# Performance work log

Measured on AMD Instinct MI355X. Metric: run time of the kernel, lower is better.

Reference implementation:

```python
import jax, jax.numpy as jnp
import numpy as np

B, C, H, W = 8, 256, 32, 32
N_HEAD, D_K, D_V, OUT_C = 8, 32, 32, 256


def _relative_indices(height, width):
    # idx[i, j] = (y_j - y_i + H) * W + (x_j - x_i + W), matching the torch loop
    ys, xs = np.meshgrid(np.arange(height), np.arange(width), indexing='ij')
    ys, xs = ys.reshape(-1), xs.reshape(-1)  # [L]
    rel_y = ys[None, :] - ys[:, None] + height  # [L, L]
    rel_x = xs[None, :] - xs[:, None] + width
    return jnp.asarray(rel_y * width + rel_x, dtype=jnp.int32)


def setup_inputs() -> dict:
    key = jax.random.key(0)
    ks = jax.random.split(key, 7)
    sc = lambda fan_in: 1.0 / np.sqrt(fan_in)
    table = ((2 * H - 1) * (2 * W - 1))  # 3969
    return {
        'x': jax.random.normal(ks[0], (B, C, H, W), jnp.float32),
        'Qw': jax.random.normal(ks[1], (C, N_HEAD * D_K), jnp.float32) * sc(C),
        'Kw': jax.random.normal(ks[2], (C, N_HEAD * D_K), jnp.float32) * sc(C),
        'Vw': jax.random.normal(ks[3], (C, N_HEAD * D_V), jnp.float32) * sc(C),
        'ffw': jax.random.normal(ks[4], (N_HEAD * D_V, OUT_C), jnp.float32) * sc(N_HEAD * D_V),
        'ffb': jax.random.normal(ks[5], (OUT_C,), jnp.float32) * 0.01,
        'rel_bias': jax.random.normal(ks[6], (N_HEAD, table), jnp.float32),
        'rel_idx': _relative_indices(H, W),  # [L, L] int32
    }


def reference(x, Qw, Kw, Vw, ffw, ffb, rel_bias, rel_idx):
    b, c, h_, w_ = x.shape
    L = h_ * w_
    nh = rel_bias.shape[0]
    dk = Qw.shape[1] // nh
    dv = Vw.shape[1] // nh
    xf = x.reshape(b, c, L).transpose(0, 2, 1)  # [b, L, c]
    q = (xf @ Qw).reshape(b, L, nh, dk).transpose(0, 2, 1, 3)  # [b, h, L, dk]
    k = (xf @ Kw).reshape(b, L, nh, dk).transpose(0, 2, 1, 3)
    v = (xf @ Vw).reshape(b, L, nh, dv).transpose(0, 2, 1, 3)
    bias = rel_bias[:, rel_idx]  # gather -> [h, L, L]
    sim = jnp.einsum('bhid,bhjd->bhij', q, k) + bias[None]  # no 1/sqrt(dk) in original
    attn = jax.nn.softmax(sim, axis=-1)  # dropout is identity in eval
    out = jnp.einsum('bhij,bhjd->bhid', attn, v)  # [b, h, L, dv]
    out = out.transpose(0, 2, 1, 3).reshape(b, L, nh * dv)
    out = out @ ffw + ffb  # [b, L, out_c]
    return out.transpose(0, 2, 1).reshape(b, -1, h_, w_)
```

## Files before the change

kernel.cpp:

```cpp
#include <hip/hip_runtime.h>
#include <math.h>


typedef unsigned short u16;
typedef __bf16 bf16;
typedef bf16 bf16x8 __attribute__((ext_vector_type(8)));
typedef bf16 bf16x4 __attribute__((ext_vector_type(4)));
typedef short s16x4 __attribute__((ext_vector_type(4)));
typedef float f32x4 __attribute__((ext_vector_type(4)));
typedef float f32x4u __attribute__((ext_vector_type(4), aligned(4)));
typedef u16 u16x8 __attribute__((ext_vector_type(8)));
typedef u16 u16x4 __attribute__((ext_vector_type(4)));

#define DEVI __device__ __forceinline__

DEVI u16 bfbits(float f) { return __builtin_bit_cast(u16, (bf16)f); }

DEVI void async_cp16(const u16* g, u16* l) {
    __builtin_amdgcn_global_load_lds((const __attribute__((address_space(1))) void*)g,
                                     (__attribute__((address_space(3))) void*)l, 16, 0, 0);
}

DEVI f32x4 pv_mfma(bf16x4 a, bf16x4 b, f32x4 c) {
#if __has_builtin(__builtin_amdgcn_mfma_f32_16x16x16bf16_1k)
    return __builtin_amdgcn_mfma_f32_16x16x16bf16_1k(
        __builtin_bit_cast(s16x4, a), __builtin_bit_cast(s16x4, b), c, 0, 0, 0);
#else
    asm("s_nop 1\n\tv_mfma_f32_16x16x16_bf16 %0, %1, %2, %0"
        : "+v"(c) : "v"(a), "v"(b));
    return c;
#endif
}

__global__ __launch_bounds__(256) void prep(const float* __restrict__ X,
                                            const float* __restrict__ Qw, const float* __restrict__ Kw,
                                            const float* __restrict__ Vw, const float* __restrict__ Fw,
                                            const float* __restrict__ RB,
                                            u16* __restrict__ XF, u16* __restrict__ WT,
                                            float* __restrict__ RBs) {
    __shared__ u16 t[64 * 65];
    const int blk = blockIdx.x, tid = threadIdx.x;
    if (blk < 576) {
        const float* src;
        int cbase, rbase, rows_total;
        u16* dst;
        if (blk < 512) {
            const int b = blk >> 6;
            cbase = (blk & 3) * 64; rbase = ((blk >> 2) & 15) * 64;
            src = X + (size_t)b * 256 * 1024; dst = XF + (size_t)b * 1024 * 256;
            rows_total = 1024;
        } else {
            const int t2 = blk - 512, wsel = t2 >> 4;
            cbase = (t2 & 3) * 64; rbase = ((t2 >> 2) & 3) * 64;
            src = wsel == 0 ? Qw : wsel == 1 ? Kw : wsel == 2 ? Vw : Fw;
            dst = WT + (size_t)wsel * 256 * 256;
            rows_total = 256;
        }
        const int w = tid >> 6, r = tid & 63;
#pragma unroll
        for (int i = 0; i < 16; i++) {
            const int c = w * 16 + i;
            t[c * 65 + r] = bfbits(src[(size_t)(cbase + c) * rows_total + rbase + r]);
        }
        __syncthreads();
#pragma unroll
        for (int i = 0; i < 2; i++) {
            const int idx = i * 256 + tid;
            const int r2 = idx >> 3, cg = idx & 7;
            u16x8 v;
#pragma unroll
            for (int j = 0; j < 8; j++) v[j] = t[(cg * 8 + j) * 65 + r2];
            *(u16x8*)&dst[(size_t)(rbase + r2) * 256 + cbase + cg * 8] = v;
        }
    } else {
        const int n = 8 * 3969;
        for (int i = (blk - 576) * 256 + tid; i < n; i += 32 * 256)
            RBs[i] = RB[i] * 1.44269504f;
    }
}

template <int MFR, int PASS>
__global__ __launch_bounds__(256, 3) void gemm_fused(const u16* __restrict__ xf, const u16* __restrict__ wt,
                                                     u16* __restrict__ q, u16* __restrict__ kk,
                                                     u16* __restrict__ vt, const u16* __restrict__ ob,
                                                     float* __restrict__ outf, const float* __restrict__ ffb) {
    constexpr int TM = MFR * 32;
    __shared__ __align__(16) u16 lA[TM * 32];
    __shared__ __align__(16) u16 lB[64 * 32];
    const int tid = threadIdx.x;
    const int wave = tid >> 6, lane = tid & 63;
    const int quad = lane >> 4, l15 = lane & 15;

    int mode, mbase, nbase;
    const u16 *A, *Bt;
    if (PASS == 2) {
        mode = 2; A = wt + 768 * 256; Bt = ob;
        mbase = (blockIdx.x & 3) * 64; nbase = (blockIdx.x >> 2) * 64;
    } else if (blockIdx.x < 512) {
        mode = 0; A = xf; Bt = wt;
        mbase = (blockIdx.x >> 3) * TM; nbase = (blockIdx.x & 7) * 64;
    } else {
        mode = 1; A = wt + 512 * 256; Bt = xf;
        const int t = blockIdx.x - 512;
        mbase = (t & 1) * TM; nbase = (t >> 1) * 64;
    }

    const int m0 = (wave >> 1) * (MFR * 16), n0 = (wave & 1) * 32;
    const int srow = tid >> 2;
    const int sgcol = (lane & 3) ^ ((lane >> 3) & 3);
    const int kcol = ((quad ^ ((l15 >> 1) & 3))) * 8;

    f32x4 acc[MFR][2];
#pragma unroll
    for (int i = 0; i < MFR; i++)
#pragma unroll
        for (int j = 0; j < 2; j++) acc[i][j] = f32x4{0.f, 0.f, 0.f, 0.f};

    for (int kb = 0; kb < 256; kb += 32) {
        __syncthreads();
#pragma unroll
        for (int half = 0; half < MFR / 2; half++)
            async_cp16(&A[(size_t)(mbase + half * 64 + srow) * 256 + kb + sgcol * 8],
                       &lA[half * 2048 + wave * 512]);
        async_cp16(&Bt[(size_t)(nbase + srow) * 256 + kb + sgcol * 8], &lB[wave * 512]);
        __syncthreads();
        bf16x8 af[MFR], bfr[2];
#pragma unroll
        for (int i = 0; i < MFR; i++) af[i] = *(const bf16x8*)&lA[(m0 + i * 16 + l15) * 32 + kcol];
#pragma unroll
        for (int j = 0; j < 2; j++) bfr[j] = *(const bf16x8*)&lB[(n0 + j * 16 + l15) * 32 + kcol];
#pragma unroll
        for (int i = 0; i < MFR; i++)
#pragma unroll
            for (int j = 0; j < 2; j++)
                acc[i][j] = __builtin_amdgcn_mfma_f32_16x16x32_bf16(af[i], bfr[j], acc[i][j], 0, 0, 0);
    }

#pragma unroll
    for (int i = 0; i < MFR; i++) {
#pragma unroll
        for (int j = 0; j < 2; j++) {
#pragma unroll
            for (int r = 0; r < 4; r++) {
                const int gm = mbase + m0 + i * 16 + quad * 4 + r;
                const int gn = nbase + n0 + j * 16 + l15;
                float v = acc[i][j][r];
                if (mode == 0) {
                    const int b = gm >> 10, l = gm & 1023;
                    int n = gn;
                    u16* dst = q;
                    if (n >= 256) { n -= 256; dst = kk; }
                    else v *= 1.44269504f;
                    const int h = n >> 5, d = n & 31;
                    dst[(((size_t)(b * 8 + h) * 1024 + l) << 5) + d] = bfbits(v);
                } else if (mode == 1) {
                    const int h = gm >> 5, d = gm & 31;
                    const int b = gn >> 10, l = gn & 1023;
                    vt[(((size_t)(b * 8 + h) * 32 + d) << 10) + l] = bfbits(v);
                } else {
                    const int b = gn >> 10, l = gn & 1023;
                    outf[(((size_t)(b * 256 + gm)) << 10) + l] = v + ffb[gm];
                }
            }
        }
    }
}

__global__ __launch_bounds__(256, 2) void attn(const u16* __restrict__ Q, const u16* __restrict__ Kb,
                                               const u16* __restrict__ Vt, const float* __restrict__ RBs,
                                               u16* __restrict__ O) {
    __shared__ __align__(16) u16 kbuf[4][2][32 * 32];
    __shared__ __align__(16) u16 vbuf[4][2][32 * 32];
    const int tid = threadIdx.x;
    const int wave = tid >> 6, lane = tid & 63;
    const int quad = lane >> 4, l15 = lane & 15;
    const int blk = blockIdx.x;
    const int bh = ((blk >> 6) << 3) + (blk & 7);
    const int qt = (blk >> 3) & 7;
    const int b = bh >> 3, h = bh & 7;
    const int qbase = qt * 128 + wave * 32;
    const size_t bhL = (size_t)bh * 1024;

    const bf16x8 qfA = *(const bf16x8*)&Q[(bhL + qbase + l15) * 32 + quad * 8];
    const bf16x8 qfB = *(const bf16x8*)&Q[(bhL + qbase + 16 + l15) * 32 + quad * 8];
    const float* brow0 = RBs + (size_t)h * 3969
                         + (32 - (qbase >> 5)) * 32 + 32 - l15 + quad * 4;
    const int srow = lane >> 2;
    const int sgcol = (lane & 3) ^ ((lane >> 3) & 3);
    const u16* ksrc = &Kb[bhL * 32];
    const u16* vsrc_lo = &Vt[(((size_t)bh * 32) + srow) << 10];
    const u16* vsrc_hi = &Vt[(((size_t)bh * 32) + 16 + srow) << 10];

    float lsumA = 0.f, lsumB = 0.f;
    f32x4 oA_lo{0.f, 0.f, 0.f, 0.f}, oA_hi{0.f, 0.f, 0.f, 0.f};
    f32x4 oB_lo{0.f, 0.f, 0.f, 0.f}, oB_hi{0.f, 0.f, 0.f, 0.f};

    const int swz = (l15 >> 1) & 3;
    const int kcol = (quad ^ swz) * 8;
    const int g0 = (2 * ((quad >> 1) ^ swz) + (quad & 1)) * 4;
    const int g1 = (2 * (((quad >> 1) + 2) ^ swz) + (quad & 1)) * 4;

#define STAGE(buf, c) do {                                                              \
        const int kb_ = (c) * 32;                                                       \
        async_cp16(ksrc + kb_ * 32 + srow * 32 + sgcol * 8, &kbuf[wave][buf][0]);       \
        async_cp16(ksrc + kb_ * 32 + 512 + srow * 32 + sgcol * 8, &kbuf[wave][buf][512]); \
        async_cp16(vsrc_lo + kb_ + sgcol * 8, &vbuf[wave][buf][0]);                     \
        async_cp16(vsrc_hi + kb_ + sgcol * 8, &vbuf[wave][buf][512]);                   \
    } while (0)

#define COMPUTE(cur, c) do {                                                              \
        const bf16x8 kf0 = *(const bf16x8*)&kbuf[wave][cur][l15 * 32 + kcol];             \
        const bf16x8 kf1 = *(const bf16x8*)&kbuf[wave][cur][(16 + l15) * 32 + kcol];      \
        const bf16x4 v00 = __builtin_bit_cast(bf16x4, *(const u16x4*)&vbuf[wave][cur][l15 * 32 + g0]); \
        const bf16x4 v10 = __builtin_bit_cast(bf16x4, *(const u16x4*)&vbuf[wave][cur][l15 * 32 + g1]); \
        const bf16x4 v01 = __builtin_bit_cast(bf16x4, *(const u16x4*)&vbuf[wave][cur][(16 + l15) * 32 + g0]); \
        const bf16x4 v11 = __builtin_bit_cast(bf16x4, *(const u16x4*)&vbuf[wave][cur][(16 + l15) * 32 + g1]); \
        const f32x4u bm = *(const f32x4u*)(brow0 + (c) * 32 - 16);                        \
        const f32x4u b0 = *(const f32x4u*)(brow0 + (c) * 32);                             \
        const f32x4u b1 = *(const f32x4u*)(brow0 + (c) * 32 + 16);                        \
        const f32x4 z{0.f, 0.f, 0.f, 0.f};                                                \
        f32x4 s0A = __builtin_amdgcn_mfma_f32_16x16x32_bf16(kf0, qfA, z, 0, 0, 0);        \
        f32x4 s1A = __builtin_amdgcn_mfma_f32_16x16x32_bf16(kf1, qfA, z, 0, 0, 0);        \
        f32x4 s0B = __builtin_amdgcn_mfma_f32_16x16x32_bf16(kf0, qfB, z, 0, 0, 0);        \
        f32x4 s1B = __builtin_amdgcn_mfma_f32_16x16x32_bf16(kf1, qfB, z, 0, 0, 0);        \
        bf16x4 p0A, p1A, p0B, p1B;                                                        \
        float lsA = 0.f, lsB = 0.f;                                                       \
        _Pragma("unroll")                                                                 \
        for (int r = 0; r < 4; r++) {                                                     \
            const float e0A = __builtin_amdgcn_exp2f(s0A[r] + b0[r]);                     \
            const float e1A = __builtin_amdgcn_exp2f(s1A[r] + b1[r]);                     \
            const float e0B = __builtin_amdgcn_exp2f(s0B[r] + bm[r]);                     \
            const float e1B = __builtin_amdgcn_exp2f(s1B[r] + b0[r]);                     \
            lsA += e0A + e1A; lsB += e0B + e1B;                                           \
            p0A[r] = (bf16)e0A; p1A[r] = (bf16)e1A;                                       \
            p0B[r] = (bf16)e0B; p1B[r] = (bf16)e1B;                                       \
        }                                                                                 \
        lsumA += lsA; lsumB += lsB;                                                       \
        oA_lo = pv_mfma(p0A, v00, oA_lo);                                                 \
        oA_hi = pv_mfma(p0A, v01, oA_hi);                                                 \
        oA_lo = pv_mfma(p1A, v10, oA_lo);                                                 \
        oA_hi = pv_mfma(p1A, v11, oA_hi);                                                 \
        oB_lo = pv_mfma(p0B, v00, oB_lo);                                                 \
        oB_hi = pv_mfma(p0B, v01, oB_hi);                                                 \
        oB_lo = pv_mfma(p1B, v10, oB_lo);                                                 \
        oB_hi = pv_mfma(p1B, v11, oB_hi);                                                 \
    } while (0)

#define WAIT4 asm volatile("s_waitcnt vmcnt(4)" ::: "memory")
#define WAIT0 asm volatile("s_waitcnt vmcnt(0)" ::: "memory")
#define DSDRAIN asm volatile("s_waitcnt lgkmcnt(0)" ::: "memory")

    STAGE(0, 0);
    STAGE(1, 1);
    for (int c = 0; c < 28; c += 2) {
        WAIT4; COMPUTE(0, c);     DSDRAIN; STAGE(0, c + 2);
        WAIT4; COMPUTE(1, c + 1); DSDRAIN; STAGE(1, c + 3);
    }
    WAIT4; COMPUTE(0, 28); DSDRAIN; STAGE(0, 30);
    WAIT4; COMPUTE(1, 29); DSDRAIN; STAGE(1, 31);
    WAIT4; COMPUTE(0, 30);
    WAIT0; COMPUTE(1, 31);
#undef STAGE
#undef COMPUTE
#undef WAIT4
#undef WAIT0
#undef DSDRAIN

    lsumA += __shfl_xor(lsumA, 16);
    lsumA += __shfl_xor(lsumA, 32);
    lsumB += __shfl_xor(lsumB, 16);
    lsumB += __shfl_xor(lsumB, 32);
#pragma unroll
    for (int r = 0; r < 4; r++) {
        const float invA = 1.f / __shfl(lsumA, quad * 4 + r);
        const float invB = 1.f / __shfl(lsumB, quad * 4 + r);
        const int iA = qbase + quad * 4 + r;
        const int iB = iA + 16;
        O[((size_t)(b * 1024 + iA) * 256) + h * 32 + l15] = bfbits(oA_lo[r] * invA);
        O[((size_t)(b * 1024 + iA) * 256) + h * 32 + 16 + l15] = bfbits(oA_hi[r] * invA);
        O[((size_t)(b * 1024 + iB) * 256) + h * 32 + l15] = bfbits(oB_lo[r] * invB);
        O[((size_t)(b * 1024 + iB) * 256) + h * 32 + 16 + l15] = bfbits(oB_hi[r] * invB);
    }
}

extern "C" void kernel_launch(void* const* d_in, const int* in_sizes, int n_in,
                              void* d_out, int out_size, void* d_ws, size_t ws_size,
                              hipStream_t stream) {
    const float* x   = (const float*)d_in[0];
    const float* Qw  = (const float*)d_in[1];
    const float* Kw  = (const float*)d_in[2];
    const float* Vw  = (const float*)d_in[3];
    const float* Fw  = (const float*)d_in[4];
    const float* ffb = (const float*)d_in[5];
    const float* RB  = (const float*)d_in[6];

    u16* ws = (u16*)d_ws;
    u16* xf = ws;
    u16* wt = xf + 2097152;
    u16* q  = wt + 262144;
    u16* kk = q  + 2097152;
    u16* vt = kk + 2097152;
    float* RBs = (float*)(vt + 2097152);
    u16* ob = xf;

    prep<<<dim3(608), 256, 0, stream>>>(x, Qw, Kw, Vw, Fw, RB, xf, wt, RBs);
    gemm_fused<4, 0><<<dim3(768), 256, 0, stream>>>(xf, wt, q, kk, vt, nullptr, nullptr, nullptr);
    attn<<<dim3(512), 256, 0, stream>>>(q, kk, vt, RBs, ob);
    gemm_fused<2, 2><<<dim3(512), 256, 0, stream>>>(xf, wt, q, kk, vt, ob, (float*)d_out, ffb);
}
```

Baseline: 117.8 us.

## Split attention key range across two wave groups and merge partials in LDS

The attention block grows from 4 to 8 waves. Each query-subtile pair of waves handles half of the 32 key chunks, and the two halves combine their output accumulators and row sums through shared memory before the final normalisation and store. This doubles the waves working on each block, adding latency hiding and parallelism for the short 512-block grid. In exchange it doubles LDS staging buffers, adds two barriers and a reduction, and each wave runs a shorter pipeline. The merge is valid without max-tracking because the softmax is computed without a running max (plain exp sums).

```diff
diff --git a/kernel.cpp b/kernel.cpp
--- a/kernel.cpp
+++ b/kernel.cpp
@@ -166,19 +166,20 @@
     }
 }
 
-__global__ __launch_bounds__(256, 2) void attn(const u16* __restrict__ Q, const u16* __restrict__ Kb,
+__global__ __launch_bounds__(512, 4) void attn(const u16* __restrict__ Q, const u16* __restrict__ Kb,
                                                const u16* __restrict__ Vt, const float* __restrict__ RBs,
                                                u16* __restrict__ O) {
-    __shared__ __align__(16) u16 kbuf[4][2][32 * 32];
-    __shared__ __align__(16) u16 vbuf[4][2][32 * 32];
+    __shared__ __align__(16) u16 kbuf[8][2][32 * 32];
+    __shared__ __align__(16) u16 vbuf[8][2][32 * 32];
     const int tid = threadIdx.x;
     const int wave = tid >> 6, lane = tid & 63;
     const int quad = lane >> 4, l15 = lane & 15;
+    const int qsub = wave & 3, half = wave >> 2;
     const int blk = blockIdx.x;
     const int bh = ((blk >> 6) << 3) + (blk & 7);
     const int qt = (blk >> 3) & 7;
     const int b = bh >> 3, h = bh & 7;
-    const int qbase = qt * 128 + wave * 32;
+    const int qbase = qt * 128 + qsub * 32;
     const size_t bhL = (size_t)bh * 1024;
 
     const bf16x8 qfA = *(const bf16x8*)&Q[(bhL + qbase + l15) * 32 + quad * 8];
@@ -250,16 +251,17 @@
 #define WAIT0 asm volatile("s_waitcnt vmcnt(0)" ::: "memory")
 #define DSDRAIN asm volatile("s_waitcnt lgkmcnt(0)" ::: "memory")
 
-    STAGE(0, 0);
-    STAGE(1, 1);
-    for (int c = 0; c < 28; c += 2) {
+    const int c0 = half * 16;
+    STAGE(0, c0);
+    STAGE(1, c0 + 1);
+    for (int c = c0; c < c0 + 12; c += 2) {
         WAIT4; COMPUTE(0, c);     DSDRAIN; STAGE(0, c + 2);
         WAIT4; COMPUTE(1, c + 1); DSDRAIN; STAGE(1, c + 3);
     }
-    WAIT4; COMPUTE(0, 28); DSDRAIN; STAGE(0, 30);
-    WAIT4; COMPUTE(1, 29); DSDRAIN; STAGE(1, 31);
-    WAIT4; COMPUTE(0, 30);
-    WAIT0; COMPUTE(1, 31);
+    WAIT4; COMPUTE(0, c0 + 12); DSDRAIN; STAGE(0, c0 + 14);
+    WAIT4; COMPUTE(1, c0 + 13); DSDRAIN; STAGE(1, c0 + 15);
+    WAIT4; COMPUTE(0, c0 + 14);
+    WAIT0; COMPUTE(1, c0 + 15);
 #undef STAGE
 #undef COMPUTE
 #undef WAIT4
@@ -270,16 +272,37 @@
     lsumA += __shfl_xor(lsumA, 32);
     lsumB += __shfl_xor(lsumB, 16);
     lsumB += __shfl_xor(lsumB, 32);
-#pragma unroll
-    for (int r = 0; r < 4; r++) {
-        const float invA = 1.f / __shfl(lsumA, quad * 4 + r);
-        const float invB = 1.f / __shfl(lsumB, quad * 4 + r);
-        const int iA = qbase + quad * 4 + r;
-        const int iB = iA + 16;
-        O[((size_t)(b * 1024 + iA) * 256) + h * 32 + l15] = bfbits(oA_lo[r] * invA);
-        O[((size_t)(b * 1024 + iA) * 256) + h * 32 + 16 + l15] = bfbits(oA_hi[r] * invA);
-        O[((size_t)(b * 1024 + iB) * 256) + h * 32 + l15] = bfbits(oB_lo[r] * invB);
-        O[((size_t)(b * 1024 + iB) * 256) + h * 32 + 16 + l15] = bfbits(oB_hi[r] * invB);
+
+    float* mg = (float*)&kbuf[0][0][0];
+    __syncthreads();
+    float* m = &mg[(qsub * 64 + lane) * 18];
+    if (half == 1) {
+#pragma unroll
+        for (int r = 0; r < 4; r++) {
+            m[r] = oA_lo[r]; m[4 + r] = oA_hi[r];
+            m[8 + r] = oB_lo[r]; m[12 + r] = oB_hi[r];
+        }
+        m[16] = lsumA; m[17] = lsumB;
+    }
+    __syncthreads();
+    if (half == 0) {
+#pragma unroll
+        for (int r = 0; r < 4; r++) {
+            oA_lo[r] += m[r]; oA_hi[r] += m[4 + r];
+            oB_lo[r] += m[8 + r]; oB_hi[r] += m[12 + r];
+        }
+        lsumA += m[16]; lsumB += m[17];
+#pragma unroll
+        for (int r = 0; r < 4; r++) {
+            const float invA = 1.f / __shfl(lsumA, quad * 4 + r);
+            const float invB = 1.f / __shfl(lsumB, quad * 4 + r);
+            const int iA = qbase + quad * 4 + r;
+            const int iB = iA + 16;
+            O[((size_t)(b * 1024 + iA) * 256) + h * 32 + l15] = bfbits(oA_lo[r] * invA);
+            O[((size_t)(b * 1024 + iA) * 256) + h * 32 + 16 + l15] = bfbits(oA_hi[r] * invA);
+            O[((size_t)(b * 1024 + iB) * 256) + h * 32 + l15] = bfbits(oB_lo[r] * invB);
+            O[((size_t)(b * 1024 + iB) * 256) + h * 32 + 16 + l15] = bfbits(oB_hi[r] * invB);
+        }
     }
 }
 
@@ -305,6 +328,6 @@
 
     prep<<<dim3(608), 256, 0, stream>>>(x, Qw, Kw, Vw, Fw, RB, xf, wt, RBs);
     gemm_fused<4, 0><<<dim3(768), 256, 0, stream>>>(xf, wt, q, kk, vt, nullptr, nullptr, nullptr);
-    attn<<<dim3(512), 256, 0, stream>>>(q, kk, vt, RBs, ob);
+    attn<<<dim3(512), 512, 0, stream>>>(q, kk, vt, RBs, ob);
     gemm_fused<2, 2><<<dim3(512), 256, 0, stream>>>(xf, wt, q, kk, vt, ob, (float*)d_out, ffb);
 }
```

Measured after the change: 131.3 us. 11.4% more time.
